# Performance work log

Measured on AMD Instinct MI355X. Metric: run time of the kernel, lower is better.

The kernel has to match this reference:

```python
import jax, jax.numpy as jnp
import numpy as np

NX, NY, NZ = 432, 496, 1
D = 64        # num_pt_features
K = 3         # NUM_K
M = 1024      # memory size
BEV = 128     # num_bev_features
NCOORD = 3
NV = 10000    # pillars in scene
NP = 16384    # points in scene
BN_EPS = 1e-3
SHRINK = 0.0025


def hard_shrink_relu(x, lambd, eps=1e-12):
    return jax.nn.relu(x - lambd) * x / (jnp.abs(x - lambd) + eps)


def batchnorm_train(x, gamma, beta, eps=BN_EPS):
    # torch BatchNorm1d training-mode math (biased variance)
    mu = jnp.mean(x, axis=0)
    var = jnp.mean((x - mu) ** 2, axis=0)
    return (x - mu) * jax.lax.rsqrt(var + eps) * gamma + beta


def pdist2(a, b, eps=1e-5):
    # sqrt(eps + |  ||a||^2 + ||b||^2 - 2 a.b |), shape [n1, n2]
    n1 = jnp.sum(a * a, axis=1, keepdims=True)
    n2 = jnp.sum(b * b, axis=1, keepdims=True)
    d2 = n1 + n2.T - 2.0 * (a @ b.T)
    return jnp.sqrt(eps + jnp.abs(d2))


def memory_lookup(x_flat, mem_w, shrink):
    # MemAE-style memory unit: softmax addressing + hard shrink + L1 renorm
    att = jax.nn.softmax(x_flat @ mem_w.T, axis=1)          # [N, M]
    att = hard_shrink_relu(att, shrink)
    att = att / jnp.maximum(jnp.sum(jnp.abs(att), axis=1, keepdims=True), 1e-12)
    return att @ mem_w                                       # [N, D]


def setup_inputs() -> dict:
    key = jax.random.key(0)
    ks = jax.random.split(key, 8)
    rng = np.random.default_rng(0)
    flat = rng.choice(NX * NY, size=NV, replace=False)       # unique BEV cells
    x = (flat % NX).astype(np.int32)
    y = (flat // NX).astype(np.int32)
    coords = jnp.asarray(np.stack([np.zeros(NV, np.int32), x, y,
                                   np.zeros(NV, np.int32)], axis=1))  # (b, x, y, z)
    pc = jax.random.uniform(ks[1], (NP, 4), dtype=jnp.float32)
    point_coords = pc * jnp.array([0.0, NX, NY, 1.0], dtype=jnp.float32)
    return {
        "pillar_features": jax.random.normal(ks[0], (NV, D), dtype=jnp.float32),
        "coords": coords,
        "point_features": jax.random.normal(ks[2], (NP, D), dtype=jnp.float32),
        "point_coords": point_coords,
        "adapt_w": jax.random.normal(ks[3], (BEV // 2, D * K), dtype=jnp.float32) * 0.05,
        "bn1_g": jnp.ones((BEV // 2,), dtype=jnp.float32),
        "bn1_b": jnp.zeros((BEV // 2,), dtype=jnp.float32),
        "weight_w": jax.random.normal(ks[4], (2, BEV // 2), dtype=jnp.float32) * 0.1,
        "bn2_g": jnp.ones((2,), dtype=jnp.float32),
        "bn2_b": jnp.zeros((2,), dtype=jnp.float32),
        "mem_w": jax.random.normal(ks[5], (M, D), dtype=jnp.float32) * 0.1,
    }


def reference(pillar_features, coords, point_features, point_coords,
              adapt_w, bn1_g, bn1_b, weight_w, bn2_g, bn2_b, mem_w):
    nv = pillar_features.shape[0]
    pillars = pillar_features.T                              # [D, nv]

    # --- coord-based retrieval: smallest-K pdist(pillar coords, point coords) ---
    dist = pdist2(coords.astype(jnp.float32), point_coords)  # [nv, np]
    _, idx_c = jax.lax.top_k(-dist, K)                       # [nv, K]
    pillars_positive_coord = point_features[idx_c]           # [nv, K, D]

    # --- feature-based retrieval: top-K of softmax(points @ pillars, axis=0) ---
    score = jax.nn.softmax(point_features @ pillars, axis=0) # [np, nv]
    _, idx_f = jax.lax.top_k(score.T, K)                     # [nv, K]
    points_positive = point_features[idx_f]                  # [nv, K, D]

    # --- memory unit on both branches ---
    out_f = memory_lookup(points_positive.reshape(nv * K, D), mem_w, SHRINK).reshape(nv, K * D)
    out_c = memory_lookup(pillars_positive_coord.reshape(nv * K, D), mem_w, SHRINK).reshape(nv, K * D)

    f = jax.nn.relu(batchnorm_train(out_f @ adapt_w.T, bn1_g, bn1_b))  # [nv, 64]
    c = jax.nn.relu(batchnorm_train(out_c @ adapt_w.T, bn1_g, bn1_b))  # [nv, 64]
    w = jax.nn.softmax(batchnorm_train(pillar_features @ weight_w.T, bn2_g, bn2_b), axis=-1)
    pillars_aug = w[:, :1] * f + w[:, 1:2] * c               # [nv, 64]
    pillars_full = jnp.concatenate([pillars, pillars_aug.T], axis=0)  # [128, nv]

    # --- scatter to BEV canvas ---
    bev_idx = coords[:, 1] + coords[:, 2] * NX + coords[:, 3]
    spatial = jnp.zeros((BEV, NX * NY), dtype=pillar_features.dtype).at[:, bev_idx].set(pillars_full)
    pind = jnp.zeros((NCOORD, NX * NY), dtype=pillar_features.dtype)
    pind = pind.at[0, bev_idx].set(coords[:, 2].astype(jnp.float32))
    pind = pind.at[1, bev_idx].set(coords[:, 3].astype(jnp.float32))
    pind = pind.at[2, bev_idx].set(coords[:, 1].astype(jnp.float32))

    spatial_features = spatial.reshape(1, BEV * NZ, NY, NX)
    spatial_indices = pind.reshape(1, NCOORD * NZ, NY, NX)
    return spatial_features, spatial_indices
```

## Files before the change

### kernel.cpp

```cpp
#include <hip/hip_runtime.h>
#include <math.h>

#define NXc 432
#define NYc 496
#define NVc 10000
#define NPc 16384
#define CELLS (NXc*NYc)
#define SHRINKc 0.0025f
#define NVPAD 10048
#define NBX 27
#define NBY 31
#define NBIN (NBX*NBY)

typedef unsigned short u16;
typedef __attribute__((ext_vector_type(8))) short s16x8;
typedef __attribute__((ext_vector_type(4))) float f32x4;

__device__ __forceinline__ unsigned med3u(unsigned a, unsigned b, unsigned c) {
    unsigned d;
    asm("v_med3_u32 %0, %1, %2, %3" : "=v"(d) : "v"(a), "v"(b), "v"(c));
    return d;
}

__device__ __forceinline__ u16 f2b(float x) {
    unsigned u = __float_as_uint(x);
    unsigned r = (u + 0x7fffu + ((u >> 16) & 1u)) >> 16;
    return (u16)r;
}

__global__ __launch_bounds__(256) void k_init(const float* __restrict__ pillar,
                                              const float* __restrict__ pfeat,
                                              const float* __restrict__ memw,
                                              const float* __restrict__ adapt,
                                              float* __restrict__ stats,
                                              int* __restrict__ cellMap,
                                              u16* __restrict__ pillarH,
                                              u16* __restrict__ pfeatH,
                                              u16* __restrict__ memwH,
                                              u16* __restrict__ memwTH,
                                              u16* __restrict__ badaptH) {
    int gid = blockIdx.x * 256 + threadIdx.x;
    if (gid < CELLS) cellMap[gid] = -1;
    if (gid < 260) stats[gid] = 0.f;
    const int N1 = NVPAD * 64;
    const int N2 = N1 + NPc * 64;
    const int N3 = N2 + 65536;
    const int N4 = N3 + 65536;
    if (gid < N1) {
        int v = gid >> 6;
        pillarH[gid] = f2b(v < NVc ? pillar[gid] : 0.f);
    } else if (gid < N2) {
        pfeatH[gid - N1] = f2b(pfeat[gid - N1]);
    } else if (gid < N3) {
        memwH[gid - N2] = f2b(memw[gid - N2]);
    } else if (gid < N4) {
        int i = gid - N3;
        int d = i >> 10, j = i & 1023;
        memwTH[i] = f2b(memw[j * 64 + d]);
    } else {
        int i = gid - N4;
        int c = i >> 6, d = i & 63;
        badaptH[i] = f2b(adapt[(c & 63) * 192 + (c >> 6) * 64 + d]);
    }
}

__global__ __launch_bounds__(1024) void k_pre(const float* __restrict__ pcoord,
                                              int* __restrict__ binStart,
                                              float4* __restrict__ binPC) {
    __shared__ int hcnt[1024];
    __shared__ int sc[1024];
    __shared__ int cur[1024];
    int t = threadIdx.x;
    hcnt[t] = 0;
    __syncthreads();
    for (int j = t; j < NPc; j += 1024) {
        float qx = pcoord[j * 4 + 1], qy = pcoord[j * 4 + 2];
        int bx = (int)(qx * 0.0625f); if (bx > NBX - 1) bx = NBX - 1;
        int by = (int)(qy * 0.0625f); if (by > NBY - 1) by = NBY - 1;
        atomicAdd(&hcnt[by * NBX + bx], 1);
    }
    __syncthreads();
    int vcount = (t < NBIN) ? hcnt[t] : 0;
    sc[t] = vcount;
    __syncthreads();
    for (int off = 1; off < 1024; off <<= 1) {
        int add = (t >= off) ? sc[t - off] : 0;
        __syncthreads();
        sc[t] += add;
        __syncthreads();
    }
    int excl = sc[t] - vcount;
    cur[t] = excl;
    if (t <= NBIN) binStart[t] = excl;
    __syncthreads();
    for (int j = t; j < NPc; j += 1024) {
        float qx = pcoord[j * 4 + 1], qy = pcoord[j * 4 + 2], qz = pcoord[j * 4 + 3];
        int bx = (int)(qx * 0.0625f); if (bx > NBX - 1) bx = NBX - 1;
        int by = (int)(qy * 0.0625f); if (by > NBY - 1) by = NBY - 1;
        int slot = atomicAdd(&cur[by * NBX + bx], 1);
        binPC[slot] = make_float4(qx, qy, qz * qz, __uint_as_float((unsigned)j));
    }
}

__global__ __launch_bounds__(256) void k_fused(const u16* __restrict__ pillarH,
                                               const u16* __restrict__ pfeatH,
                                               const u16* __restrict__ memwH,
                                               const u16* __restrict__ memwTH,
                                               const int* __restrict__ coords,
                                               const float4* __restrict__ binPC,
                                               const int* __restrict__ binStart,
                                               u16* __restrict__ PoutH,
                                               int* __restrict__ dIdx6,
                                               int* __restrict__ sIdx) {
    __shared__ union {
        u16 bf[8192];
        struct { u16 wh[4096]; u16 wt[4096]; u16 st[4][1024]; } m;
    } smem;
    int bid = blockIdx.x;
    int t = threadIdx.x;
    int w = t >> 6, l = t & 63;
    int lm = l & 15, qd = l >> 4;

    if (bid < 256) {
        int pb = bid * 64;
        u16* WH = smem.m.wh;
        u16* WT = smem.m.wt;
        u16* ST = &smem.m.st[w][0];
        const u16* arow = pfeatH + (size_t)(pb + 16 * w + lm) * 64 + qd * 8;
        s16x8 a0 = *(const s16x8*)arow;
        s16x8 a1 = *(const s16x8*)(arow + 32);
        float mM[4] = {-INFINITY, -INFINITY, -INFINITY, -INFINITY};
        float Zs[4] = {0.f, 0.f, 0.f, 0.f};
        for (int tile = 0; tile < 16; ++tile) {
            __syncthreads();
#pragma unroll
            for (int r = 0; r < 2; ++r) {
                int q = t + 256 * r;
                int row = q >> 3, g = q & 7;
                uint4 v = *(const uint4*)(memwH + (size_t)(tile * 64 + row) * 64 + g * 8);
                *(uint4*)&WH[(((row >> 4) * 8 + g) * 16 + ((row & 15) ^ g)) * 8] = v;
            }
            __syncthreads();
            f32x4 acc[4];
#pragma unroll
            for (int st = 0; st < 4; ++st) {
                s16x8 b0 = *(const s16x8*)&WH[((st * 8 + qd) * 16 + (lm ^ qd)) * 8];
                s16x8 b1 = *(const s16x8*)&WH[((st * 8 + qd + 4) * 16 + (lm ^ (qd + 4))) * 8];
                f32x4 z = {0.f, 0.f, 0.f, 0.f};
                z = __builtin_amdgcn_mfma_f32_16x16x32_bf16(a0, b0, z, 0, 0, 0);
                z = __builtin_amdgcn_mfma_f32_16x16x32_bf16(a1, b1, z, 0, 0, 0);
                acc[st] = z;
            }
#pragma unroll
            for (int r = 0; r < 4; ++r) {
                float tmax = acc[0][r];
#pragma unroll
                for (int st = 1; st < 4; ++st) tmax = fmaxf(tmax, acc[st][r]);
                float mn = fmaxf(mM[r], tmax);
                float zacc = Zs[r] * __expf(mM[r] - mn);
#pragma unroll
                for (int st = 0; st < 4; ++st) zacc += __expf(acc[st][r] - mn);
                mM[r] = mn; Zs[r] = zacc;
            }
        }
#pragma unroll
        for (int r = 0; r < 4; ++r) {
#pragma unroll
            for (int off = 1; off < 16; off <<= 1) {
                float om = __shfl_xor(mM[r], off);
                float oz = __shfl_xor(Zs[r], off);
                float mn = fmaxf(mM[r], om);
                Zs[r] = Zs[r] * __expf(mM[r] - mn) + oz * __expf(om - mn);
                mM[r] = mn;
            }
        }
        float invZ[4], L1[4] = {0.f, 0.f, 0.f, 0.f};
#pragma unroll
        for (int r = 0; r < 4; ++r) invZ[r] = 1.f / Zs[r];
        f32x4 oacc[4];
#pragma unroll
        for (int n = 0; n < 4; ++n) oacc[n] = (f32x4){0.f, 0.f, 0.f, 0.f};
        for (int tile = 0; tile < 16; ++tile) {
            __syncthreads();
#pragma unroll
            for (int r = 0; r < 2; ++r) {
                int q = t + 256 * r;
                int row = q >> 3, g = q & 7;
                uint4 v = *(const uint4*)(memwH + (size_t)(tile * 64 + row) * 64 + g * 8);
                *(uint4*)&WH[(((row >> 4) * 8 + g) * 16 + ((row & 15) ^ g)) * 8] = v;
            }
#pragma unroll
            for (int r = 0; r < 2; ++r) {
                int q = t + 256 * r;
                int row = q >> 3, g = q & 7;
                uint4 v = *(const uint4*)(memwTH + (size_t)row * 1024 + tile * 64 + g * 8);
                *(uint4*)&WT[(g * 64 + (row ^ g)) * 8] = v;
            }
            __syncthreads();
#pragma unroll
            for (int st = 0; st < 4; ++st) {
                s16x8 b0 = *(const s16x8*)&WH[((st * 8 + qd) * 16 + (lm ^ qd)) * 8];
                s16x8 b1 = *(const s16x8*)&WH[((st * 8 + qd + 4) * 16 + (lm ^ (qd + 4))) * 8];
                f32x4 z = {0.f, 0.f, 0.f, 0.f};
                z = __builtin_amdgcn_mfma_f32_16x16x32_bf16(a0, b0, z, 0, 0, 0);
                z = __builtin_amdgcn_mfma_f32_16x16x32_bf16(a1, b1, z, 0, 0, 0);
                int g2 = st * 2 + (lm >> 3);
#pragma unroll
                for (int r = 0; r < 4; ++r) {
                    float e = __expf(z[r] - mM[r]);
                    float a = e * invZ[r];
                    float tt = a - SHRINKc;
                    float sres = fmaxf(tt, 0.f) * a / (fabsf(tt) + 1e-12f);
                    L1[r] += sres;
                    int rr = qd * 4 + r;
                    ST[(g2 * 16 + (rr ^ g2)) * 8 + (lm & 7)] = f2b(sres);
                }
            }
#pragma unroll
            for (int ks = 0; ks < 2; ++ks) {
                int g = ks * 4 + qd;
                s16x8 af = *(const s16x8*)&ST[(g * 16 + (lm ^ g)) * 8];
#pragma unroll
                for (int n = 0; n < 4; ++n) {
                    s16x8 bf = *(const s16x8*)&WT[(g * 64 + ((n * 16 + lm) ^ g)) * 8];
                    oacc[n] = __builtin_amdgcn_mfma_f32_16x16x32_bf16(af, bf, oacc[n], 0, 0, 0);
                }
            }
        }
#pragma unroll
        for (int r = 0; r < 4; ++r) {
#pragma unroll
            for (int off = 1; off < 16; off <<= 1) L1[r] += __shfl_xor(L1[r], off);
            L1[r] = 1.f / fmaxf(L1[r], 1e-12f);
        }
#pragma unroll
        for (int n = 0; n < 4; ++n)
#pragma unroll
            for (int r = 0; r < 4; ++r)
                PoutH[(size_t)(pb + 16 * w + qd * 4 + r) * 64 + n * 16 + lm] =
                    f2b(oacc[n][r] * L1[r]);
    } else if (bid < 296) {
        int v = (bid - 256) * 256 + t;
        if (v >= NVc) return;
        int xi = coords[v * 4 + 1], yi = coords[v * 4 + 2];
        float x = (float)xi, y = (float)yi;
        int bx = xi >> 4; if (bx > NBX - 1) bx = NBX - 1;
        int by = yi >> 4; if (by > NBY - 1) by = NBY - 1;
        unsigned kk[6] = {~0u, ~0u, ~0u, ~0u, ~0u, ~0u};
        for (int r = 0; r < 32; ++r) {
            int x0 = bx - r, x1 = bx + r, y0 = by - r, y1 = by + r;
            for (int cy = y0; cy <= y1; ++cy) {
                if (cy < 0 || cy > NBY - 1) continue;
                int step = (cy == y0 || cy == y1) ? 1 : (x1 > x0 ? x1 - x0 : 1);
                for (int cx = x0; cx <= x1; cx += step) {
                    if (cx < 0 || cx > NBX - 1) continue;
                    int b = cy * NBX + cx;
                    int s0 = binStart[b], s1 = binStart[b + 1];
                    for (int s = s0; s < s1; ++s) {
                        float4 p = binPC[s];
                        float e1 = x - p.x, e2 = y - p.y;
                        float d2 = fmaf(e1, e1, fmaf(e2, e2, p.z));
                        unsigned tk = (__float_as_uint(d2) & 0xFFFFC000u) | __float_as_uint(p.w);
                        kk[5] = med3u(kk[4], kk[5], tk);
                        kk[4] = med3u(kk[3], kk[4], tk);
                        kk[3] = med3u(kk[2], kk[3], tk);
                        kk[2] = med3u(kk[1], kk[2], tk);
                        kk[1] = med3u(kk[0], kk[1], tk);
                        kk[0] = kk[0] < tk ? kk[0] : tk;
                    }
                }
            }
            if (kk[2] != ~0u) {
                float d3 = __uint_as_float(kk[2] & 0xFFFFC000u);
                if (256.f * (float)(r * r) > d3 * 1.004f + 1e-3f) break;
            }
        }
#pragma unroll
        for (int j2 = 0; j2 < 6; ++j2) dIdx6[v * 6 + j2] = (int)(kk[j2] & 16383u);
    } else {
        int sb = bid - 296;
        int pb = (sb >> 4) * 64;
        int cb = (sb & 15) * 1024;
        const u16* arow = pillarH + (size_t)(pb + 16 * w + lm) * 64 + qd * 8;
        s16x8 a0 = *(const s16x8*)arow;
        s16x8 a1 = *(const s16x8*)(arow + 32);
        int so[4], doff[4];
#pragma unroll
        for (int r = 0; r < 4; ++r) {
            int q = t + 256 * r;
            int row = q >> 3, g = q & 7;
            so[r] = row * 64 + g * 8;
            doff[r] = (((row >> 4) * 8 + g) * 16 + ((row & 15) ^ g)) * 8;
        }
        const u16* src = pfeatH + (size_t)cb * 64;
        unsigned sk[4][4];
#pragma unroll
        for (int r = 0; r < 4; ++r)
#pragma unroll
            for (int j = 0; j < 4; ++j) sk[r][j] = 0u;
        for (int s = 0; s < 8; ++s) {
            const u16* s2 = src + (size_t)s * 128 * 64;
#pragma unroll
            for (int r = 0; r < 4; ++r)
                *(uint4*)&smem.bf[doff[r]] = *(const uint4*)(s2 + so[r]);
            __syncthreads();
#pragma unroll
            for (int pt = 0; pt < 8; ++pt) {
                s16x8 b0 = *(const s16x8*)&smem.bf[(((pt * 8 + qd) * 16) + (lm ^ qd)) * 8];
                s16x8 b1 = *(const s16x8*)&smem.bf[(((pt * 8 + qd + 4) * 16) + (lm ^ (qd + 4))) * 8];
                f32x4 acc = {256.f, 256.f, 256.f, 256.f};
                acc = __builtin_amdgcn_mfma_f32_16x16x32_bf16(a0, b0, acc, 0, 0, 0);
                acc = __builtin_amdgcn_mfma_f32_16x16x32_bf16(a1, b1, acc, 0, 0, 0);
                unsigned idf = (unsigned)(1023 - (s * 128 + pt * 16 + lm));
#pragma unroll
                for (int r = 0; r < 4; ++r) {
                    unsigned key = (__float_as_uint(acc[r]) & 0xFFFFFC00u) | idf;
                    sk[r][3] = med3u(sk[r][2], sk[r][3], key);
                    sk[r][2] = med3u(sk[r][1], sk[r][2], key);
                    sk[r][1] = med3u(sk[r][0], sk[r][1], key);
                    sk[r][0] = sk[r][0] > key ? sk[r][0] : key;
                }
            }
            __syncthreads();
        }
        unsigned* mrg = (unsigned*)&smem.bf[0];
#pragma unroll
        for (int r = 0; r < 4; ++r) {
            int row = 16 * w + qd * 4 + r;
            *(uint4*)&mrg[(row * 16 + lm) * 4] =
                make_uint4(sk[r][0], sk[r][1], sk[r][2], sk[r][3]);
        }
        __syncthreads();
        if (t < 64) {
            int gpr = pb + t;
            unsigned m0 = 0u, m1 = 0u, m2 = 0u, m3 = 0u;
#pragma unroll 4
            for (int cc = 0; cc < 16; ++cc) {
                uint4 v = *(const uint4*)&mrg[(t * 16 + cc) * 4];
#pragma unroll
                for (int j = 0; j < 4; ++j) {
                    unsigned x = j == 0 ? v.x : (j == 1 ? v.y : (j == 2 ? v.z : v.w));
                    m3 = med3u(m2, m3, x);
                    m2 = med3u(m1, m2, x);
                    m1 = med3u(m0, m1, x);
                    m0 = m0 > x ? m0 : x;
                }
            }
            if (gpr < NVc) {
                int base = ((sb & 15) * NVc + gpr) * 4;
                sIdx[base + 0] = cb + 1023 - (int)(m0 & 1023u);
                sIdx[base + 1] = cb + 1023 - (int)(m1 & 1023u);
                sIdx[base + 2] = cb + 1023 - (int)(m2 & 1023u);
                sIdx[base + 3] = cb + 1023 - (int)(m3 & 1023u);
            }
        }
    }
}

__global__ __launch_bounds__(256) void k_fused2(const u16* __restrict__ PoutH,
                                                const u16* __restrict__ badaptH,
                                                const float* __restrict__ pillar,
                                                const int* __restrict__ coords,
                                                const float* __restrict__ pfeat,
                                                const float* __restrict__ pcoord,
                                                const int* __restrict__ sIdx,
                                                const int* __restrict__ dIdx6,
                                                float* __restrict__ Q,
                                                int* __restrict__ idx_f,
                                                int* __restrict__ idx_c) {
    __shared__ u16 AD[12288];
    int bid = blockIdx.x;
    int t = threadIdx.x;
    if (bid < 256) {
        int w = t >> 6, l = t & 63;
        int lm = l & 15, qd = l >> 4;
        int pb = bid * 64;
#pragma unroll
        for (int r = 0; r < 6; ++r) {
            int q = t + 256 * r;
            int row = q >> 3, g = q & 7;
            uint4 v = *(const uint4*)(badaptH + (size_t)row * 64 + g * 8);
            *(uint4*)&AD[(((row >> 4) * 8 + g) * 16 + ((row & 15) ^ g)) * 8] = v;
        }
        const u16* arow = PoutH + (size_t)(pb + 16 * w + lm) * 64 + qd * 8;
        s16x8 a0 = *(const s16x8*)arow;
        s16x8 a1 = *(const s16x8*)(arow + 32);
        __syncthreads();
        f32x4 acc[12];
#pragma unroll
        for (int nt = 0; nt < 12; ++nt) {
            s16x8 b0 = *(const s16x8*)&AD[(((nt * 8 + qd) * 16) + (lm ^ qd)) * 8];
            s16x8 b1 = *(const s16x8*)&AD[(((nt * 8 + qd + 4) * 16) + (lm ^ (qd + 4))) * 8];
            f32x4 z = {0.f, 0.f, 0.f, 0.f};
            z = __builtin_amdgcn_mfma_f32_16x16x32_bf16(a0, b0, z, 0, 0, 0);
            z = __builtin_amdgcn_mfma_f32_16x16x32_bf16(a1, b1, z, 0, 0, 0);
            acc[nt] = z;
        }
#pragma unroll
        for (int nt = 0; nt < 12; ++nt)
#pragma unroll
            for (int r = 0; r < 4; ++r)
                Q[(size_t)(pb + 16 * w + qd * 4 + r) * 192 + nt * 16 + lm] = acc[nt][r];
    } else {
        int wv = t >> 6, l = t & 63;
        int v = (bid - 256) * 4 + wv;
        int chunk = l >> 2, slot = l & 3;
        int ps = sIdx[(chunk * NVc + v) * 4 + slot];
        int pd = dIdx6[v * 6 + (l < 6 ? l : 0)];
        double s = 0.0;
#pragma unroll
        for (int i = 0; i < 16; ++i) {
            float4 a = *(const float4*)(pillar + v * 64 + 4 * i);
            float4 b = *(const float4*)(pfeat + ps * 64 + 4 * i);
            s += (double)a.x * (double)b.x + (double)a.y * (double)b.y
               + (double)a.z * (double)b.z + (double)a.w * (double)b.w;
        }
        float4 qc = *(const float4*)(pcoord + pd * 4);
        double db_ = (double)coords[v * 4 + 0] - (double)qc.x;
        double dx_ = (double)coords[v * 4 + 1] - (double)qc.y;
        double dy_ = (double)coords[v * 4 + 2] - (double)qc.z;
        double dz_ = (double)coords[v * 4 + 3] - (double)qc.w;
        double d2 = db_ * db_ + dx_ * dx_ + dy_ * dy_ + dz_ * dz_;
        double sv = s; int sx = ps;
        for (int k = 0; k < 3; ++k) {
            double bv = sv; int bi = sx;
#pragma unroll
            for (int off = 32; off >= 1; off >>= 1) {
                double ov = __shfl_xor(bv, off);
                int    oi = __shfl_xor(bi, off);
                if (ov > bv || (ov == bv && oi < bi)) { bv = ov; bi = oi; }
            }
            if (l == 0) idx_f[v * 3 + k] = bi;
            if (sx == bi) { sv = -INFINITY; sx = 0x7fffffff; }
        }
        double dv = d2; int dx2 = pd;
        for (int k = 0; k < 3; ++k) {
            double bv = dv; int bi = dx2;
#pragma unroll
            for (int off = 32; off >= 1; off >>= 1) {
                double ov = __shfl_xor(bv, off);
                int    oi = __shfl_xor(bi, off);
                if (ov < bv || (ov == bv && oi < bi)) { bv = ov; bi = oi; }
            }
            if (l == 0) idx_c[v * 3 + k] = bi;
            if (dx2 == bi) { dv = INFINITY; dx2 = 0x7fffffff; }
        }
    }
}

__global__ __launch_bounds__(256) void k_gather(const float* __restrict__ Q,
                                                const int* __restrict__ idx_f,
                                                const int* __restrict__ idx_c,
                                                const float* __restrict__ pillar,
                                                const int* __restrict__ coords,
                                                const float* __restrict__ ww,
                                                float* __restrict__ f_pre,
                                                float* __restrict__ c_pre,
                                                float* __restrict__ w_pre,
                                                float* __restrict__ stats,
                                                int* __restrict__ cellMap) {
    __shared__ float red[4][4][64];
    __shared__ float redw[4][4];
    int t = threadIdx.x;
    int wv = t >> 6, l = t & 63;
    int base = blockIdx.x * 40;
    int vend = base + 40;
    if (t < 40) {
        int v = base + t;
        int cell = coords[v * 4 + 1] + coords[v * 4 + 2] * NXc + coords[v * 4 + 3];
        cellMap[cell] = v;
    }
    float fs = 0, fq = 0, cs = 0, cq = 0, ws0 = 0, wq0 = 0, ws1 = 0, wq1 = 0;
    float w0l = ww[l], w1l = ww[64 + l];
    for (int v = base + wv; v < vend; v += 4) {
        int if0 = idx_f[v * 3], if1 = idx_f[v * 3 + 1], if2 = idx_f[v * 3 + 2];
        float f = Q[if0 * 192 + l] + Q[if1 * 192 + 64 + l] + Q[if2 * 192 + 128 + l];
        f_pre[v * 64 + l] = f; fs += f; fq += f * f;
        int ic0 = idx_c[v * 3], ic1 = idx_c[v * 3 + 1], ic2 = idx_c[v * 3 + 2];
        float c = Q[ic0 * 192 + l] + Q[ic1 * 192 + 64 + l] + Q[ic2 * 192 + 128 + l];
        c_pre[v * 64 + l] = c; cs += c; cq += c * c;
        float pv = pillar[v * 64 + l];
        float a0 = pv * w0l, a1 = pv * w1l;
#pragma unroll
        for (int off = 32; off >= 1; off >>= 1) {
            a0 += __shfl_xor(a0, off);
            a1 += __shfl_xor(a1, off);
        }
        if (l == 0) { w_pre[v * 2] = a0; w_pre[v * 2 + 1] = a1; }
        ws0 += a0; wq0 += a0 * a0; ws1 += a1; wq1 += a1 * a1;
    }
    red[0][wv][l] = fs; red[1][wv][l] = fq; red[2][wv][l] = cs; red[3][wv][l] = cq;
    if (l == 0) { redw[wv][0] = ws0; redw[wv][1] = wq0; redw[wv][2] = ws1; redw[wv][3] = wq1; }
    __syncthreads();
    if (wv == 0) {
#pragma unroll
        for (int q = 0; q < 4; ++q) {
            float sum = red[q][0][l] + red[q][1][l] + red[q][2][l] + red[q][3][l];
            atomicAdd(&stats[q * 64 + l], sum);
        }
        if (l < 4) {
            float sum = redw[0][l] + redw[1][l] + redw[2][l] + redw[3][l];
            atomicAdd(&stats[256 + l], sum);
        }
    }
}

__global__ __launch_bounds__(256) void k_out2(const int* __restrict__ cellMap,
                                              const float* __restrict__ pillar,
                                              const float* __restrict__ f_pre,
                                              const float* __restrict__ c_pre,
                                              const float* __restrict__ w_pre,
                                              const float* __restrict__ stats,
                                              const float* __restrict__ g1,
                                              const float* __restrict__ b1,
                                              const float* __restrict__ g2,
                                              const float* __restrict__ b2,
                                              float* __restrict__ out) {
    int c4 = (blockIdx.x * 256 + threadIdx.x) * 4;
    if (c4 >= CELLS) return;
    int4 cm = *(const int4*)(cellMap + c4);
    const float invn = 1.0f / (float)NVc;
    float mw0 = stats[256] * invn, vw0 = stats[257] * invn - mw0 * mw0;
    float mw1 = stats[258] * invn, vw1 = stats[259] * invn - mw1 * mw1;
    float rw0 = rsqrtf(vw0 + 1e-3f), rw1 = rsqrtf(vw1 + 1e-3f);
    float g20 = g2[0], b20 = b2[0], g21 = g2[1], b21 = b2[1];
    float w0c[4], w1c[4];
    int cms[4] = {cm.x, cm.y, cm.z, cm.w};
#pragma unroll
    for (int k = 0; k < 4; ++k) {
        int c = cms[k];
        if (c >= 0) {
            float z0 = (w_pre[c * 2] - mw0) * rw0 * g20 + b20;
            float z1 = (w_pre[c * 2 + 1] - mw1) * rw1 * g21 + b21;
            float mz = fmaxf(z0, z1);
            float e0 = __expf(z0 - mz), e1 = __expf(z1 - mz);
            float wd = 1.f / (e0 + e1);
            w0c[k] = e0 * wd; w1c[k] = e1 * wd;
        } else { w0c[k] = 0.f; w1c[k] = 0.f; }
    }
    int f0 = blockIdx.y * 33;
    int f1 = f0 + 33; if (f1 > 131) f1 = 131;
    for (int f = f0; f < f1; ++f) {
        float4 val;
        if (f < 64) {
            val.x = cm.x >= 0 ? pillar[cm.x * 64 + f] : 0.f;
            val.y = cm.y >= 0 ? pillar[cm.y * 64 + f] : 0.f;
            val.z = cm.z >= 0 ? pillar[cm.z * 64 + f] : 0.f;
            val.w = cm.w >= 0 ? pillar[cm.w * 64 + f] : 0.f;
        } else if (f < 128) {
            int fa = f - 64;
            float mf = stats[fa] * invn;
            float rf = rsqrtf(stats[64 + fa] * invn - mf * mf + 1e-3f);
            float mc = stats[128 + fa] * invn;
            float rc = rsqrtf(stats[192 + fa] * invn - mc * mc + 1e-3f);
            float gg = g1[fa], bb = b1[fa];
            float* vv = (float*)&val;
#pragma unroll
            for (int k = 0; k < 4; ++k) {
                int c = cms[k];
                if (c >= 0) {
                    float fv = fmaxf((f_pre[c * 64 + fa] - mf) * rf * gg + bb, 0.f);
                    float cv = fmaxf((c_pre[c * 64 + fa] - mc) * rc * gg + bb, 0.f);
                    vv[k] = w0c[k] * fv + w1c[k] * cv;
                } else vv[k] = 0.f;
            }
        } else if (f == 128) {
            val.x = cm.x >= 0 ? (float)((c4 + 0) / NXc) : 0.f;
            val.y = cm.y >= 0 ? (float)((c4 + 1) / NXc) : 0.f;
            val.z = cm.z >= 0 ? (float)((c4 + 2) / NXc) : 0.f;
            val.w = cm.w >= 0 ? (float)((c4 + 3) / NXc) : 0.f;
        } else if (f == 129) {
            val = make_float4(0.f, 0.f, 0.f, 0.f);
        } else {
            val.x = cm.x >= 0 ? (float)((c4 + 0) % NXc) : 0.f;
            val.y = cm.y >= 0 ? (float)((c4 + 1) % NXc) : 0.f;
            val.z = cm.z >= 0 ? (float)((c4 + 2) % NXc) : 0.f;
            val.w = cm.w >= 0 ? (float)((c4 + 3) % NXc) : 0.f;
        }
        *(float4*)(out + (size_t)f * CELLS + c4) = val;
    }
}

extern "C" void kernel_launch(void* const* d_in, const int* in_sizes, int n_in,
                              void* d_out, int out_size, void* d_ws, size_t ws_size,
                              hipStream_t stream) {
    const float* pillar = (const float*)d_in[0];
    const int*   coords = (const int*)d_in[1];
    const float* pfeat  = (const float*)d_in[2];
    const float* pcoord = (const float*)d_in[3];
    const float* adapt  = (const float*)d_in[4];
    const float* bn1g   = (const float*)d_in[5];
    const float* bn1b   = (const float*)d_in[6];
    const float* ww     = (const float*)d_in[7];
    const float* bn2g   = (const float*)d_in[8];
    const float* bn2b   = (const float*)d_in[9];
    const float* memw   = (const float*)d_in[10];
    float* out = (float*)d_out;
    float* ws  = (float*)d_ws;
    u16*   PoutH = (u16*)(ws + 0);
    float* Q     = ws + 1048576;
    int*   sIdx  = (int*)(ws + 4194304);
    int*   binStart  = (int*)(ws + 4834304);
    int*   dIdx6     = (int*)(ws + 4836824);
    float4* binPC    = (float4*)(ws + 4896824);
    u16*   memwH   = (u16*)(ws + 4970000);
    u16*   memwTH  = (u16*)(ws + 5002768);
    u16*   badaptH = (u16*)(ws + 5035536);
    int*   idxf  = (int*)(ws + 5474304);
    int*   idxc  = (int*)(ws + 5504304);
    float* fpre  = ws + 5534304;
    float* cpre  = ws + 6174304;
    float* wpre  = ws + 6814304;
    float* stats = ws + 6834304;
    int*   cellMap = (int*)(ws + 6840000);
    u16* pillarH = (u16*)(ws + 5534304);
    u16* pfeatH  = pillarH + (size_t)NVPAD * 64;

    k_init  <<<7168, 256, 0, stream>>>(pillar, pfeat, memw, adapt, stats, cellMap,
                                       pillarH, pfeatH, memwH, memwTH, badaptH);
    k_pre   <<<1, 1024, 0, stream>>>(pcoord, binStart, binPC);
    k_fused <<<2808, 256, 0, stream>>>(pillarH, pfeatH, memwH, memwTH, coords,
                                       binPC, binStart, PoutH, dIdx6, sIdx);
    k_fused2<<<2756, 256, 0, stream>>>(PoutH, badaptH, pillar, coords, pfeat, pcoord,
                                       sIdx, dIdx6, Q, idxf, idxc);
    k_gather<<<250, 256, 0, stream>>>(Q, idxf, idxc, pillar, coords, ww,
                                      fpre, cpre, wpre, stats, cellMap);
    k_out2  <<<dim3(210, 4), 256, 0, stream>>>(cellMap, pillar, fpre, cpre, wpre, stats,
                                               bn1g, bn1b, bn2g, bn2b, out);
}
```

Baseline: 323.4 us.

## Load MFMA B-operands directly from global memory instead of LDS staging

Removes the shared-memory staging of memory weights, transposed weights, point features and adapt weights across the fused kernels. Each wave now loads its MFMA B fragments straight from global memory, relying on L1/L2 caching, which eliminates block-wide barriers and LDS writes. The top-4 merge in the KNN branch is also changed from an LDS scratch pass plus a single-wave merge to a shuffle-based in-register merge across the 16 lanes. The cost is more global and cache traffic, since each of the four waves in a block reloads the same B data, and more latency exposed on every MFMA.

Result: slower. 461.0 us (+42.5%).

```diff
diff --git a/kernel.cpp b/kernel.cpp
--- a/kernel.cpp
+++ b/kernel.cpp
@@ -112,10 +112,7 @@
                                                u16* __restrict__ PoutH,
                                                int* __restrict__ dIdx6,
                                                int* __restrict__ sIdx) {
-    __shared__ union {
-        u16 bf[8192];
-        struct { u16 wh[4096]; u16 wt[4096]; u16 st[4][1024]; } m;
-    } smem;
+    __shared__ u16 STbuf[4][1024];
     int bid = blockIdx.x;
     int t = threadIdx.x;
     int w = t >> 6, l = t & 63;
@@ -123,29 +120,19 @@
 
     if (bid < 256) {
         int pb = bid * 64;
-        u16* WH = smem.m.wh;
-        u16* WT = smem.m.wt;
-        u16* ST = &smem.m.st[w][0];
+        u16* ST = &STbuf[w][0];
         const u16* arow = pfeatH + (size_t)(pb + 16 * w + lm) * 64 + qd * 8;
         s16x8 a0 = *(const s16x8*)arow;
         s16x8 a1 = *(const s16x8*)(arow + 32);
         float mM[4] = {-INFINITY, -INFINITY, -INFINITY, -INFINITY};
         float Zs[4] = {0.f, 0.f, 0.f, 0.f};
         for (int tile = 0; tile < 16; ++tile) {
-            __syncthreads();
-#pragma unroll
-            for (int r = 0; r < 2; ++r) {
-                int q = t + 256 * r;
-                int row = q >> 3, g = q & 7;
-                uint4 v = *(const uint4*)(memwH + (size_t)(tile * 64 + row) * 64 + g * 8);
-                *(uint4*)&WH[(((row >> 4) * 8 + g) * 16 + ((row & 15) ^ g)) * 8] = v;
-            }
-            __syncthreads();
             f32x4 acc[4];
 #pragma unroll
             for (int st = 0; st < 4; ++st) {
-                s16x8 b0 = *(const s16x8*)&WH[((st * 8 + qd) * 16 + (lm ^ qd)) * 8];
-                s16x8 b1 = *(const s16x8*)&WH[((st * 8 + qd + 4) * 16 + (lm ^ (qd + 4))) * 8];
+                const u16* brow = memwH + (size_t)(tile * 64 + st * 16 + lm) * 64 + qd * 8;
+                s16x8 b0 = *(const s16x8*)brow;
+                s16x8 b1 = *(const s16x8*)(brow + 32);
                 f32x4 z = {0.f, 0.f, 0.f, 0.f};
                 z = __builtin_amdgcn_mfma_f32_16x16x32_bf16(a0, b0, z, 0, 0, 0);
                 z = __builtin_amdgcn_mfma_f32_16x16x32_bf16(a1, b1, z, 0, 0, 0);
@@ -181,26 +168,11 @@
 #pragma unroll
         for (int n = 0; n < 4; ++n) oacc[n] = (f32x4){0.f, 0.f, 0.f, 0.f};
         for (int tile = 0; tile < 16; ++tile) {
-            __syncthreads();
-#pragma unroll
-            for (int r = 0; r < 2; ++r) {
-                int q = t + 256 * r;
-                int row = q >> 3, g = q & 7;
-                uint4 v = *(const uint4*)(memwH + (size_t)(tile * 64 + row) * 64 + g * 8);
-                *(uint4*)&WH[(((row >> 4) * 8 + g) * 16 + ((row & 15) ^ g)) * 8] = v;
-            }
-#pragma unroll
-            for (int r = 0; r < 2; ++r) {
-                int q = t + 256 * r;
-                int row = q >> 3, g = q & 7;
-                uint4 v = *(const uint4*)(memwTH + (size_t)row * 1024 + tile * 64 + g * 8);
-                *(uint4*)&WT[(g * 64 + (row ^ g)) * 8] = v;
-            }
-            __syncthreads();
 #pragma unroll
             for (int st = 0; st < 4; ++st) {
-                s16x8 b0 = *(const s16x8*)&WH[((st * 8 + qd) * 16 + (lm ^ qd)) * 8];
-                s16x8 b1 = *(const s16x8*)&WH[((st * 8 + qd + 4) * 16 + (lm ^ (qd + 4))) * 8];
+                const u16* brow = memwH + (size_t)(tile * 64 + st * 16 + lm) * 64 + qd * 8;
+                s16x8 b0 = *(const s16x8*)brow;
+                s16x8 b1 = *(const s16x8*)(brow + 32);
                 f32x4 z = {0.f, 0.f, 0.f, 0.f};
                 z = __builtin_amdgcn_mfma_f32_16x16x32_bf16(a0, b0, z, 0, 0, 0);
                 z = __builtin_amdgcn_mfma_f32_16x16x32_bf16(a1, b1, z, 0, 0, 0);
@@ -222,7 +194,8 @@
                 s16x8 af = *(const s16x8*)&ST[(g * 16 + (lm ^ g)) * 8];
 #pragma unroll
                 for (int n = 0; n < 4; ++n) {
-                    s16x8 bf = *(const s16x8*)&WT[(g * 64 + ((n * 16 + lm) ^ g)) * 8];
+                    s16x8 bf = *(const s16x8*)(memwTH
+                        + (size_t)(n * 16 + lm) * 1024 + tile * 64 + g * 8);
                     oacc[n] = __builtin_amdgcn_mfma_f32_16x16x32_bf16(af, bf, oacc[n], 0, 0, 0);
                 }
             }
@@ -284,30 +257,18 @@
         const u16* arow = pillarH + (size_t)(pb + 16 * w + lm) * 64 + qd * 8;
         s16x8 a0 = *(const s16x8*)arow;
         s16x8 a1 = *(const s16x8*)(arow + 32);
-        int so[4], doff[4];
-#pragma unroll
-        for (int r = 0; r < 4; ++r) {
-            int q = t + 256 * r;
-            int row = q >> 3, g = q & 7;
-            so[r] = row * 64 + g * 8;
-            doff[r] = (((row >> 4) * 8 + g) * 16 + ((row & 15) ^ g)) * 8;
-        }
-        const u16* src = pfeatH + (size_t)cb * 64;
         unsigned sk[4][4];
 #pragma unroll
         for (int r = 0; r < 4; ++r)
 #pragma unroll
             for (int j = 0; j < 4; ++j) sk[r][j] = 0u;
         for (int s = 0; s < 8; ++s) {
-            const u16* s2 = src + (size_t)s * 128 * 64;
-#pragma unroll
-            for (int r = 0; r < 4; ++r)
-                *(uint4*)&smem.bf[doff[r]] = *(const uint4*)(s2 + so[r]);
-            __syncthreads();
+            const u16* base = pfeatH + (size_t)(cb + s * 128) * 64;
 #pragma unroll
             for (int pt = 0; pt < 8; ++pt) {
-                s16x8 b0 = *(const s16x8*)&smem.bf[(((pt * 8 + qd) * 16) + (lm ^ qd)) * 8];
-                s16x8 b1 = *(const s16x8*)&smem.bf[(((pt * 8 + qd + 4) * 16) + (lm ^ (qd + 4))) * 8];
+                const u16* brow = base + (size_t)(pt * 16 + lm) * 64 + qd * 8;
+                s16x8 b0 = *(const s16x8*)brow;
+                s16x8 b1 = *(const s16x8*)(brow + 32);
                 f32x4 acc = {256.f, 256.f, 256.f, 256.f};
                 acc = __builtin_amdgcn_mfma_f32_16x16x32_bf16(a0, b0, acc, 0, 0, 0);
                 acc = __builtin_amdgcn_mfma_f32_16x16x32_bf16(a1, b1, acc, 0, 0, 0);
@@ -321,37 +282,46 @@
                     sk[r][0] = sk[r][0] > key ? sk[r][0] : key;
                 }
             }
-            __syncthreads();
-        }
-        unsigned* mrg = (unsigned*)&smem.bf[0];
-#pragma unroll
-        for (int r = 0; r < 4; ++r) {
-            int row = 16 * w + qd * 4 + r;
-            *(uint4*)&mrg[(row * 16 + lm) * 4] =
-                make_uint4(sk[r][0], sk[r][1], sk[r][2], sk[r][3]);
-        }
-        __syncthreads();
-        if (t < 64) {
-            int gpr = pb + t;
-            unsigned m0 = 0u, m1 = 0u, m2 = 0u, m3 = 0u;
-#pragma unroll 4
-            for (int cc = 0; cc < 16; ++cc) {
-                uint4 v = *(const uint4*)&mrg[(t * 16 + cc) * 4];
-#pragma unroll
-                for (int j = 0; j < 4; ++j) {
-                    unsigned x = j == 0 ? v.x : (j == 1 ? v.y : (j == 2 ? v.z : v.w));
-                    m3 = med3u(m2, m3, x);
-                    m2 = med3u(m1, m2, x);
-                    m1 = med3u(m0, m1, x);
-                    m0 = m0 > x ? m0 : x;
+        }
+#pragma unroll
+        for (int off = 1; off < 16; off <<= 1) {
+#pragma unroll
+            for (int r = 0; r < 4; ++r) {
+                unsigned o0 = __shfl_xor(sk[r][0], off);
+                unsigned o1 = __shfl_xor(sk[r][1], off);
+                unsigned o2 = __shfl_xor(sk[r][2], off);
+                unsigned o3 = __shfl_xor(sk[r][3], off);
+                sk[r][3] = med3u(sk[r][2], sk[r][3], o0);
+                sk[r][2] = med3u(sk[r][1], sk[r][2], o0);
+                sk[r][1] = med3u(sk[r][0], sk[r][1], o0);
+                sk[r][0] = sk[r][0] > o0 ? sk[r][0] : o0;
+                sk[r][3] = med3u(sk[r][2], sk[r][3], o1);
+                sk[r][2] = med3u(sk[r][1], sk[r][2], o1);
+                sk[r][1] = med3u(sk[r][0], sk[r][1], o1);
+                sk[r][0] = sk[r][0] > o1 ? sk[r][0] : o1;
+                sk[r][3] = med3u(sk[r][2], sk[r][3], o2);
+                sk[r][2] = med3u(sk[r][1], sk[r][2], o2);
+                sk[r][1] = med3u(sk[r][0], sk[r][1], o2);
+                sk[r][0] = sk[r][0] > o2 ? sk[r][0] : o2;
+                sk[r][3] = med3u(sk[r][2], sk[r][3], o3);
+                sk[r][2] = med3u(sk[r][1], sk[r][2], o3);
+                sk[r][1] = med3u(sk[r][0], sk[r][1], o3);
+                sk[r][0] = sk[r][0] > o3 ? sk[r][0] : o3;
+            }
+        }
+        if (lm == 0) {
+            int chunk = sb & 15;
+#pragma unroll
+            for (int r = 0; r < 4; ++r) {
+                int gpr = pb + 16 * w + qd * 4 + r;
+                if (gpr < NVc) {
+                    int4 v;
+                    v.x = cb + 1023 - (int)(sk[r][0] & 1023u);
+                    v.y = cb + 1023 - (int)(sk[r][1] & 1023u);
+                    v.z = cb + 1023 - (int)(sk[r][2] & 1023u);
+                    v.w = cb + 1023 - (int)(sk[r][3] & 1023u);
+                    *(int4*)&sIdx[(chunk * NVc + gpr) * 4] = v;
                 }
-            }
-            if (gpr < NVc) {
-                int base = ((sb & 15) * NVc + gpr) * 4;
-                sIdx[base + 0] = cb + 1023 - (int)(m0 & 1023u);
-                sIdx[base + 1] = cb + 1023 - (int)(m1 & 1023u);
-                sIdx[base + 2] = cb + 1023 - (int)(m2 & 1023u);
-                sIdx[base + 3] = cb + 1023 - (int)(m3 & 1023u);
             }
         }
     }
@@ -368,29 +338,21 @@
                                                 float* __restrict__ Q,
                                                 int* __restrict__ idx_f,
                                                 int* __restrict__ idx_c) {
-    __shared__ u16 AD[12288];
     int bid = blockIdx.x;
     int t = threadIdx.x;
     if (bid < 256) {
         int w = t >> 6, l = t & 63;
         int lm = l & 15, qd = l >> 4;
         int pb = bid * 64;
-#pragma unroll
-        for (int r = 0; r < 6; ++r) {
-            int q = t + 256 * r;
-            int row = q >> 3, g = q & 7;
-            uint4 v = *(const uint4*)(badaptH + (size_t)row * 64 + g * 8);
-            *(uint4*)&AD[(((row >> 4) * 8 + g) * 16 + ((row & 15) ^ g)) * 8] = v;
-        }
         const u16* arow = PoutH + (size_t)(pb + 16 * w + lm) * 64 + qd * 8;
         s16x8 a0 = *(const s16x8*)arow;
         s16x8 a1 = *(const s16x8*)(arow + 32);
-        __syncthreads();
         f32x4 acc[12];
 #pragma unroll
         for (int nt = 0; nt < 12; ++nt) {
-            s16x8 b0 = *(const s16x8*)&AD[(((nt * 8 + qd) * 16) + (lm ^ qd)) * 8];
-            s16x8 b1 = *(const s16x8*)&AD[(((nt * 8 + qd + 4) * 16) + (lm ^ (qd + 4))) * 8];
+            const u16* brow = badaptH + (size_t)(nt * 16 + lm) * 64 + qd * 8;
+            s16x8 b0 = *(const s16x8*)brow;
+            s16x8 b1 = *(const s16x8*)(brow + 32);
             f32x4 z = {0.f, 0.f, 0.f, 0.f};
             z = __builtin_amdgcn_mfma_f32_16x16x32_bf16(a0, b0, z, 0, 0, 0);
             z = __builtin_amdgcn_mfma_f32_16x16x32_bf16(a1, b1, z, 0, 0, 0);
```

## Double-buffer point-feature tiles and merge top-4 via wave shuffles

Applied to the files above, without the earlier changes.

In the pillar-to-point top-k branch, the shared tile buffer becomes double-buffered. The next 128-point chunk is loaded into registers before the MFMA work on the current chunk and written to the other buffer afterwards, which removes one barrier per iteration and overlaps global loads with compute. The final per-row top-4 merge now uses xor shuffles across the 16 lanes instead of a shared-memory round trip followed by a single-wave serial merge, and results are written as int4 stores. This doubles the shared buffer size, which may affect occupancy, and adds extra registers for prefetch.

Result: no change. 323.7 us (+0.1%).

```diff
diff --git a/kernel.cpp b/kernel.cpp
--- a/kernel.cpp
+++ b/kernel.cpp
@@ -113,7 +113,7 @@
                                                int* __restrict__ dIdx6,
                                                int* __restrict__ sIdx) {
     __shared__ union {
-        u16 bf[8192];
+        u16 bf[2][8192];
         struct { u16 wh[4096]; u16 wt[4096]; u16 st[4][1024]; } m;
     } smem;
     int bid = blockIdx.x;
@@ -292,22 +292,29 @@
             so[r] = row * 64 + g * 8;
             doff[r] = (((row >> 4) * 8 + g) * 16 + ((row & 15) ^ g)) * 8;
         }
+        uint4 pre[4];
         const u16* src = pfeatH + (size_t)cb * 64;
+#pragma unroll
+        for (int r = 0; r < 4; ++r) pre[r] = *(const uint4*)(src + so[r]);
+#pragma unroll
+        for (int r = 0; r < 4; ++r) *(uint4*)&smem.bf[0][doff[r]] = pre[r];
         unsigned sk[4][4];
 #pragma unroll
         for (int r = 0; r < 4; ++r)
 #pragma unroll
             for (int j = 0; j < 4; ++j) sk[r][j] = 0u;
         for (int s = 0; s < 8; ++s) {
-            const u16* s2 = src + (size_t)s * 128 * 64;
-#pragma unroll
-            for (int r = 0; r < 4; ++r)
-                *(uint4*)&smem.bf[doff[r]] = *(const uint4*)(s2 + so[r]);
             __syncthreads();
+            if (s < 7) {
+                const u16* s2 = src + (size_t)(s + 1) * 128 * 64;
+#pragma unroll
+                for (int r = 0; r < 4; ++r) pre[r] = *(const uint4*)(s2 + so[r]);
+            }
+            const u16* B = &smem.bf[s & 1][0];
 #pragma unroll
             for (int pt = 0; pt < 8; ++pt) {
-                s16x8 b0 = *(const s16x8*)&smem.bf[(((pt * 8 + qd) * 16) + (lm ^ qd)) * 8];
-                s16x8 b1 = *(const s16x8*)&smem.bf[(((pt * 8 + qd + 4) * 16) + (lm ^ (qd + 4))) * 8];
+                s16x8 b0 = *(const s16x8*)&B[(((pt * 8 + qd) * 16) + (lm ^ qd)) * 8];
+                s16x8 b1 = *(const s16x8*)&B[(((pt * 8 + qd + 4) * 16) + (lm ^ (qd + 4))) * 8];
                 f32x4 acc = {256.f, 256.f, 256.f, 256.f};
                 acc = __builtin_amdgcn_mfma_f32_16x16x32_bf16(a0, b0, acc, 0, 0, 0);
                 acc = __builtin_amdgcn_mfma_f32_16x16x32_bf16(a1, b1, acc, 0, 0, 0);
@@ -321,37 +328,50 @@
                     sk[r][0] = sk[r][0] > key ? sk[r][0] : key;
                 }
             }
-            __syncthreads();
-        }
-        unsigned* mrg = (unsigned*)&smem.bf[0];
-#pragma unroll
-        for (int r = 0; r < 4; ++r) {
-            int row = 16 * w + qd * 4 + r;
-            *(uint4*)&mrg[(row * 16 + lm) * 4] =
-                make_uint4(sk[r][0], sk[r][1], sk[r][2], sk[r][3]);
-        }
-        __syncthreads();
-        if (t < 64) {
-            int gpr = pb + t;
-            unsigned m0 = 0u, m1 = 0u, m2 = 0u, m3 = 0u;
-#pragma unroll 4
-            for (int cc = 0; cc < 16; ++cc) {
-                uint4 v = *(const uint4*)&mrg[(t * 16 + cc) * 4];
-#pragma unroll
-                for (int j = 0; j < 4; ++j) {
-                    unsigned x = j == 0 ? v.x : (j == 1 ? v.y : (j == 2 ? v.z : v.w));
-                    m3 = med3u(m2, m3, x);
-                    m2 = med3u(m1, m2, x);
-                    m1 = med3u(m0, m1, x);
-                    m0 = m0 > x ? m0 : x;
+            if (s < 7) {
+#pragma unroll
+                for (int r = 0; r < 4; ++r) *(uint4*)&smem.bf[(s + 1) & 1][doff[r]] = pre[r];
+            }
+        }
+#pragma unroll
+        for (int off = 1; off < 16; off <<= 1) {
+#pragma unroll
+            for (int r = 0; r < 4; ++r) {
+                unsigned o0 = __shfl_xor(sk[r][0], off);
+                unsigned o1 = __shfl_xor(sk[r][1], off);
+                unsigned o2 = __shfl_xor(sk[r][2], off);
+                unsigned o3 = __shfl_xor(sk[r][3], off);
+                sk[r][3] = med3u(sk[r][2], sk[r][3], o0);
+                sk[r][2] = med3u(sk[r][1], sk[r][2], o0);
+                sk[r][1] = med3u(sk[r][0], sk[r][1], o0);
+                sk[r][0] = sk[r][0] > o0 ? sk[r][0] : o0;
+                sk[r][3] = med3u(sk[r][2], sk[r][3], o1);
+                sk[r][2] = med3u(sk[r][1], sk[r][2], o1);
+                sk[r][1] = med3u(sk[r][0], sk[r][1], o1);
+                sk[r][0] = sk[r][0] > o1 ? sk[r][0] : o1;
+                sk[r][3] = med3u(sk[r][2], sk[r][3], o2);
+                sk[r][2] = med3u(sk[r][1], sk[r][2], o2);
+                sk[r][1] = med3u(sk[r][0], sk[r][1], o2);
+                sk[r][0] = sk[r][0] > o2 ? sk[r][0] : o2;
+                sk[r][3] = med3u(sk[r][2], sk[r][3], o3);
+                sk[r][2] = med3u(sk[r][1], sk[r][2], o3);
+                sk[r][1] = med3u(sk[r][0], sk[r][1], o3);
+                sk[r][0] = sk[r][0] > o3 ? sk[r][0] : o3;
+            }
+        }
+        if (lm == 0) {
+            int chunk = sb & 15;
+#pragma unroll
+            for (int r = 0; r < 4; ++r) {
+                int gpr = pb + 16 * w + qd * 4 + r;
+                if (gpr < NVc) {
+                    int4 v;
+                    v.x = cb + 1023 - (int)(sk[r][0] & 1023u);
+                    v.y = cb + 1023 - (int)(sk[r][1] & 1023u);
+                    v.z = cb + 1023 - (int)(sk[r][2] & 1023u);
+                    v.w = cb + 1023 - (int)(sk[r][3] & 1023u);
+                    *(int4*)&sIdx[(chunk * NVc + gpr) * 4] = v;
                 }
-            }
-            if (gpr < NVc) {
-                int base = ((sb & 15) * NVc + gpr) * 4;
-                sIdx[base + 0] = cb + 1023 - (int)(m0 & 1023u);
-                sIdx[base + 1] = cb + 1023 - (int)(m1 & 1023u);
-                sIdx[base + 2] = cb + 1023 - (int)(m2 & 1023u);
-                sIdx[base + 3] = cb + 1023 - (int)(m3 & 1023u);
             }
         }
     }
```
